# Performance work log

Hardware: AMD Instinct MI355X
Metric: run time of the kernel (lower is better)

The kernel has to match this reference:

```python
import jax, jax.numpy as jnp
import numpy as np

B, L1, L2 = 4, 2048, 2048
INP1_DIM = INP2_DIM = 1024
QK_DIM = V_DIM = 1024
HEAD_N = 16
QK_HEAD = QK_DIM // HEAD_N  # 64
V_HEAD = V_DIM // HEAD_N    # 64
SCALE = 1.0 / (QK_HEAD ** 0.5)


def _linear_params(key, out_dim, in_dim):
    # torch nn.Linear default init: U(-1/sqrt(in), 1/sqrt(in)) for W and b
    kw, kb = jax.random.split(key)
    bound = 1.0 / np.sqrt(in_dim)
    W = jax.random.uniform(kw, (out_dim, in_dim), jnp.float32, -bound, bound)
    b = jax.random.uniform(kb, (out_dim,), jnp.float32, -bound, bound)
    return W, b


def setup_inputs() -> dict:
    key = jax.random.key(0)
    k1, k2, kq, kk, kv = jax.random.split(key, 5)
    inp1 = jax.random.normal(k1, (B, L1, INP1_DIM), jnp.float32)
    inp2 = jax.random.normal(k2, (B, L2, INP2_DIM), jnp.float32)
    Wq, bq = _linear_params(kq, QK_DIM, INP1_DIM)
    Wk, bk = _linear_params(kk, QK_DIM, INP2_DIM)
    Wv, bv = _linear_params(kv, V_DIM, INP2_DIM)
    return {"inp1": inp1, "inp2": inp2, "Wq": Wq, "bq": bq,
            "Wk": Wk, "bk": bk, "Wv": Wv, "bv": bv,
            "rescale_with_score": 1}


def reference(inp1, inp2, Wq, bq, Wk, bk, Wv, bv, rescale_with_score):
    b, l1, _ = inp1.shape
    l2 = inp2.shape[1]
    # torch Linear: x @ W.T + b
    q = (jnp.einsum('bld,ed->ble', inp1, Wq) + bq).reshape(b, l1, HEAD_N, QK_HEAD)
    k = (jnp.einsum('bmd,ed->bme', inp2, Wk) + bk).reshape(b, l2, HEAD_N, QK_HEAD)
    v = (jnp.einsum('bmd,ed->bme', inp2, Wv) + bv).reshape(b, l2, HEAD_N, V_HEAD)
    # scores: [b, l1, l2, h], softmax over l2 (axis=2)
    s = jax.nn.softmax(jnp.einsum('blhd,bmhd->blmh', q, k) * SCALE, axis=2)
    res = jnp.einsum('blmh,bmhd->blhd', s, v)  # [b, l1, h, v_head]
    if rescale_with_score:
        # per-query, per-head sum of squared attention weights -> [b, l1, h, 1]
        denom = jnp.sqrt(jnp.sum(s * s, axis=2))[..., None]
        res = res / denom
    return res.reshape(b, l1, -1)
```

## Files before the change

### kernel.cpp

```cpp
#include <hip/hip_runtime.h>
#include <hip/hip_bf16.h>

#define HEADS   16
#define HD      64
#define DMODEL  1024
#define LQ      2048
#define LK      2048
#define BATCH   4
#define MROWS   8192

typedef __attribute__((ext_vector_type(8))) short short8;
typedef __attribute__((ext_vector_type(4))) float f32x4;
typedef __attribute__((ext_vector_type(16))) float f32x16;
typedef __attribute__((ext_vector_type(2))) unsigned int uint2v;

union V4u { unsigned u[4]; short8 s8; };

static __device__ __forceinline__ unsigned short f2bf(float f) {
  unsigned u = __builtin_bit_cast(unsigned, f);
  u = (u + 0x7FFFu + ((u >> 16) & 1u)) >> 16;
  return (unsigned short)u;
}

static __device__ __forceinline__ unsigned cvtpk(float lo, float hi) {
  unsigned w;
  asm("v_cvt_pk_bf16_f32 %0, %1, %2" : "=v"(w) : "v"(lo), "v"(hi));
  return w;
}

static __device__ __forceinline__ void permswap(unsigned &a, unsigned &b) {
  asm volatile("v_permlane32_swap_b32 %0, %1" : "+v"(a), "+v"(b));
}

static __device__ __forceinline__ void gload_lds16(const void* g, void* l) {
  __builtin_amdgcn_global_load_lds(
      (const __attribute__((address_space(1))) unsigned int*)g,
      (__attribute__((address_space(3))) unsigned int*)l, 16, 0, 0);
}

static __device__ __forceinline__ unsigned lds_addr(const void* p) {
  return (unsigned)(size_t)(const __attribute__((address_space(3))) void*)p;
}

static __device__ __forceinline__ void ds_read128(unsigned addr, V4u &d) {
  asm volatile("ds_read_b128 %0, %1" : "=v"(d.s8) : "v"(addr));
}

static __device__ __forceinline__ void ds_read_tr(unsigned addr, uint2v &d) {
  asm volatile("ds_read_b64_tr_b16 %0, %1" : "=v"(d) : "v"(addr));
}

__global__ void cvt_in_kernel(const float* __restrict__ s0, unsigned short* __restrict__ d0,
                              const float* __restrict__ s1, unsigned short* __restrict__ d1,
                              int n4) {
  int i = blockIdx.x * blockDim.x + threadIdx.x;
  if (i >= n4) return;
  const float* s = blockIdx.y ? s1 : s0;
  unsigned short* d = blockIdx.y ? d1 : d0;
  float4 v = ((const float4*)s)[i];
  ushort4 o;
  o.x = f2bf(v.x); o.y = f2bf(v.y); o.z = f2bf(v.z); o.w = f2bf(v.w);
  ((ushort4*)d)[i] = o;
}

__global__ void cvt_w_kernel(const float* __restrict__ s0, unsigned short* __restrict__ d0,
                             const float* __restrict__ s1, unsigned short* __restrict__ d1,
                             const float* __restrict__ s2, unsigned short* __restrict__ d2,
                             float scale0, int n4) {
  int i = blockIdx.x * blockDim.x + threadIdx.x;
  if (i >= n4) return;
  const float* s = blockIdx.y == 0 ? s0 : (blockIdx.y == 1 ? s1 : s2);
  unsigned short* d = blockIdx.y == 0 ? d0 : (blockIdx.y == 1 ? d1 : d2);
  float sc = blockIdx.y == 0 ? scale0 : 1.0f;
  float4 v = ((const float4*)s)[i];
  ushort4 o;
  o.x = f2bf(v.x * sc); o.y = f2bf(v.y * sc); o.z = f2bf(v.z * sc); o.w = f2bf(v.w * sc);
  ((ushort4*)d)[i] = o;
}

__global__ __launch_bounds__(256, 4) void gemm3_kernel(
    const unsigned short* __restrict__ X1,
    const unsigned short* __restrict__ X2,
    const unsigned short* __restrict__ Wqb,
    const unsigned short* __restrict__ Wkb,
    const unsigned short* __restrict__ Wvb,
    const float* __restrict__ bq,
    const float* __restrict__ bk,
    const float* __restrict__ bv,
    unsigned short* __restrict__ Qb,
    unsigned short* __restrict__ Kb,
    unsigned short* __restrict__ Vb,
    float cexp) {
  __shared__ __attribute__((aligned(16))) unsigned short As[128 * 32];
  __shared__ __attribute__((aligned(16))) unsigned short Bs[128 * 32];
  const int sel = blockIdx.z;
  const unsigned short* A = (sel == 0) ? X1 : X2;
  const unsigned short* W = (sel == 0) ? Wqb : (sel == 1) ? Wkb : Wvb;
  const float* bias = (sel == 0) ? bq : (sel == 1) ? bk : bv;
  unsigned short* C = (sel == 0) ? Qb : (sel == 1) ? Kb : Vb;
  const float bscale = (sel == 0) ? cexp : 1.0f;

  const int tid = threadIdx.x;
  const int l = tid & 63, w = tid >> 6;
  const int c = l & 15, g = l >> 4;
  const int wm = w >> 1, wn = w & 1;
  const int m0 = blockIdx.x * 128, n0 = blockIdx.y * 128;

  f32x4 acc[4][4];
#pragma unroll
  for (int i = 0; i < 4; ++i)
#pragma unroll
    for (int j = 0; j < 4; ++j) acc[i][j] = (f32x4){0.f, 0.f, 0.f, 0.f};

  for (int k0 = 0; k0 < 1024; k0 += 32) {
#pragma unroll
    for (int is = 0; is < 2; ++is) {
      int lin = is * 256 + tid;
      int r = lin >> 2, s = lin & 3;
      int gofs = (s ^ (r & 3)) * 8;
      gload_lds16(A + (size_t)(m0 + r) * 1024 + k0 + gofs,
                  &As[(is * 256 + (tid & ~63)) * 8]);
      gload_lds16(W + (size_t)(n0 + r) * 1024 + k0 + gofs,
                  &Bs[(is * 256 + (tid & ~63)) * 8]);
    }
    __syncthreads();
    short8 af[4], bfr[4];
#pragma unroll
    for (int mt = 0; mt < 4; ++mt) {
      int row = wm * 64 + mt * 16 + c;
      af[mt] = *(const short8*)((const char*)As + row * 64 + ((g ^ (row & 3)) << 4));
    }
#pragma unroll
    for (int nt = 0; nt < 4; ++nt) {
      int row = wn * 64 + nt * 16 + c;
      bfr[nt] = *(const short8*)((const char*)Bs + row * 64 + ((g ^ (row & 3)) << 4));
    }
    __builtin_amdgcn_s_setprio(1);
#pragma unroll
    for (int mt = 0; mt < 4; ++mt)
#pragma unroll
      for (int nt = 0; nt < 4; ++nt)
        acc[mt][nt] = __builtin_amdgcn_mfma_f32_16x16x32_bf16(af[mt], bfr[nt], acc[mt][nt], 0, 0, 0);
    __builtin_amdgcn_s_setprio(0);
    __syncthreads();
  }
  float bv4[4];
#pragma unroll
  for (int nt = 0; nt < 4; ++nt) bv4[nt] = bias[n0 + wn * 64 + nt * 16 + c] * bscale;
#pragma unroll
  for (int mt = 0; mt < 4; ++mt)
#pragma unroll
    for (int nt = 0; nt < 4; ++nt)
#pragma unroll
      for (int r = 0; r < 4; ++r) {
        int m = m0 + wm * 64 + mt * 16 + g * 4 + r;
        int n = n0 + wn * 64 + nt * 16 + c;
        C[(size_t)m * 1024 + n] = f2bf(acc[mt][nt][r] + bv4[nt]);
      }
}

__global__ __launch_bounds__(512) void attn_kernel(
    const unsigned short* __restrict__ Q,
    const unsigned short* __restrict__ K,
    const unsigned short* __restrict__ V,
    float* __restrict__ out,
    const int* __restrict__ rescale_flag) {
  __shared__ __attribute__((aligned(16))) unsigned short Kbuf[2][64 * 64];
  __shared__ __attribute__((aligned(16))) unsigned short Vbuf[2][64 * 64];
  __shared__ float ivLds[8][32];

  const int tid = threadIdx.x;
  const int lane = tid & 63, w = tid >> 6;
  const int l31 = lane & 31, hi = lane >> 5;

  const int gid = blockIdx.x;
  const int xcd = gid & 7;
  const int o = gid >> 3;
  const int bh = xcd * 8 + (o >> 3);
  const int qb = o & 7;
  const int bb = bh >> 4, h = bh & 15;
  const size_t qrowb = (size_t)bb * LQ + qb * 256 + w * 32;

  const int rs = *rescale_flag;

  short8 qf[4];
#pragma unroll
  for (int ks = 0; ks < 4; ++ks)
    qf[ks] = *(const short8*)(Q + (qrowb + l31) * 1024 + h * 64 + ks * 16 + hi * 8);

  const size_t kvbase = (size_t)bb * LK * 1024 + (size_t)h * 64;
  const int k_kv = w * 8 + (lane >> 3);
  const int k_sl = (lane & 7) ^ (lane >> 3);
  const unsigned short* ksrc0 = K + kvbase + (size_t)k_kv * 1024 + k_sl * 8;
  const int v_kv = (w & 3) * 16 + ((lane >> 4) & 1) * 8 + ((lane >> 5) & 1) * 4 + ((lane >> 1) & 3);
  const int v_d  = (w >> 2) * 32 + ((lane >> 3) & 1) * 16 + (lane & 1) * 8;
  const unsigned short* vsrc0 = V + kvbase + (size_t)v_kv * 1024 + v_d;

  unsigned koff[4];
#pragma unroll
  for (int ks = 0; ks < 4; ++ks)
    koff[ks] = (unsigned)(l31 * 128 + ((((ks << 1) | hi) ^ (l31 & 7)) << 4));
  const unsigned kbase0 = lds_addr(&Kbuf[0][0]);
  const unsigned vbase0 = lds_addr(&Vbuf[0][0]);

  f32x16 po[2];
  po[0] = {}; po[1] = {};
  float zacc0 = 0.f, zacc1 = 0.f, s2acc0 = 0.f, s2acc1 = 0.f;

  gload_lds16(ksrc0, &Kbuf[0][w * 512]);
  gload_lds16(vsrc0, &Vbuf[0][w * 512]);
  __syncthreads();

  int cur = 0;
  for (int t = 0; t < LK / 64; ++t) {
    if (t < LK / 64 - 1) {
      gload_lds16(ksrc0 + (size_t)(t + 1) * 65536, &Kbuf[cur ^ 1][w * 512]);
      gload_lds16(vsrc0 + (size_t)(t + 1) * 65536, &Vbuf[cur ^ 1][w * 512]);
    }
    const unsigned kb = kbase0 + (unsigned)(cur * 8192);
    const unsigned vtr = vbase0 + (unsigned)(cur * 8192) + (unsigned)(lane * 8);

#pragma unroll
    for (int s = 0; s < 2; ++s) {
      V4u kfr[4];
#pragma unroll
      for (int ks = 0; ks < 4; ++ks) ds_read128(kb + s * 4096 + koff[ks], kfr[ks]);
      uint2v ta0, ta1, ta2, ta3, tb0, tb1, tb2, tb3;
      {
        const unsigned a0r = vtr + (2 * s) * 1024;
        const unsigned a1r = vtr + (2 * s + 1) * 1024;
        ds_read_tr(a0r, ta0);
        ds_read_tr(a0r + 512, ta1);
        ds_read_tr(a0r + 4096, ta2);
        ds_read_tr(a0r + 4096 + 512, ta3);
        ds_read_tr(a1r, tb0);
        ds_read_tr(a1r + 512, tb1);
        ds_read_tr(a1r + 4096, tb2);
        ds_read_tr(a1r + 4096 + 512, tb3);
      }
      asm volatile("s_waitcnt lgkmcnt(8)" ::: "memory");
      __builtin_amdgcn_sched_barrier(0);
      f32x16 ps = {};
      __builtin_amdgcn_s_setprio(1);
#pragma unroll
      for (int ks = 0; ks < 4; ++ks)
        ps = __builtin_amdgcn_mfma_f32_32x32x16_bf16(kfr[ks].s8, qf[ks], ps, 0, 0, 0);
      __builtin_amdgcn_s_setprio(0);
      float p[16];
#pragma unroll
      for (int r = 0; r < 16; ++r) p[r] = __builtin_amdgcn_exp2f(ps[r]);
      if (rs) {
#pragma unroll
        for (int r = 0; r < 8; ++r) {
          s2acc0 = fmaf(p[2 * r], p[2 * r], s2acc0);
          s2acc1 = fmaf(p[2 * r + 1], p[2 * r + 1], s2acc1);
        }
      } else {
#pragma unroll
        for (int r = 0; r < 8; ++r) {
          zacc0 += p[2 * r];
          zacc1 += p[2 * r + 1];
        }
      }
      unsigned wlo[4], whi[4];
#pragma unroll
      for (int b = 0; b < 4; ++b) {
        wlo[b] = cvtpk(p[4 * b + 0], p[4 * b + 1]);
        whi[b] = cvtpk(p[4 * b + 2], p[4 * b + 3]);
      }
      {
        unsigned a0 = wlo[0], b0 = wlo[1];
        unsigned a1 = whi[0], b1 = whi[1];
        permswap(a0, b0);
        permswap(a1, b1);
        V4u pau; pau.u[0] = a0; pau.u[1] = a1; pau.u[2] = b0; pau.u[3] = b1;
        asm volatile("s_waitcnt lgkmcnt(4)" ::: "memory");
        __builtin_amdgcn_sched_barrier(0);
        V4u v0u, v1u;
        v0u.u[0] = ta0[0]; v0u.u[1] = ta0[1]; v0u.u[2] = ta1[0]; v0u.u[3] = ta1[1];
        v1u.u[0] = ta2[0]; v1u.u[1] = ta2[1]; v1u.u[2] = ta3[0]; v1u.u[3] = ta3[1];
        __builtin_amdgcn_s_setprio(1);
        po[0] = __builtin_amdgcn_mfma_f32_32x32x16_bf16(pau.s8, v0u.s8, po[0], 0, 0, 0);
        po[1] = __builtin_amdgcn_mfma_f32_32x32x16_bf16(pau.s8, v1u.s8, po[1], 0, 0, 0);
        __builtin_amdgcn_s_setprio(0);
      }
      {
        unsigned a0 = wlo[2], b0 = wlo[3];
        unsigned a1 = whi[2], b1 = whi[3];
        permswap(a0, b0);
        permswap(a1, b1);
        V4u pau; pau.u[0] = a0; pau.u[1] = a1; pau.u[2] = b0; pau.u[3] = b1;
        asm volatile("s_waitcnt lgkmcnt(0)" ::: "memory");
        __builtin_amdgcn_sched_barrier(0);
        V4u v0u, v1u;
        v0u.u[0] = tb0[0]; v0u.u[1] = tb0[1]; v0u.u[2] = tb1[0]; v0u.u[3] = tb1[1];
        v1u.u[0] = tb2[0]; v1u.u[1] = tb2[1]; v1u.u[2] = tb3[0]; v1u.u[3] = tb3[1];
        __builtin_amdgcn_s_setprio(1);
        po[0] = __builtin_amdgcn_mfma_f32_32x32x16_bf16(pau.s8, v0u.s8, po[0], 0, 0, 0);
        po[1] = __builtin_amdgcn_mfma_f32_32x32x16_bf16(pau.s8, v1u.s8, po[1], 0, 0, 0);
        __builtin_amdgcn_s_setprio(0);
      }
    }
    __syncthreads();
    cur ^= 1;
  }

  float zacc = zacc0 + zacc1, s2acc = s2acc0 + s2acc1;
  float z2 = zacc + __shfl_xor(zacc, 32, 64);
  float s22 = s2acc + __shfl_xor(s2acc, 32, 64);
  float iv = rs ? (1.0f / sqrtf(s22)) : (1.0f / z2);
  ivLds[w][l31] = iv;

#pragma unroll
  for (int dt = 0; dt < 2; ++dt)
#pragma unroll
    for (int r = 0; r < 16; ++r) {
      const int ql = (r & 3) + 8 * (r >> 2) + 4 * hi;
      out[(qrowb + ql) * 1024 + h * 64 + dt * 32 + l31] = po[dt][r] * ivLds[w][ql];
    }
}

extern "C" void kernel_launch(void* const* d_in, const int* in_sizes, int n_in,
                              void* d_out, int out_size, void* d_ws, size_t ws_size,
                              hipStream_t stream) {
  const float* inp1 = (const float*)d_in[0];
  const float* inp2 = (const float*)d_in[1];
  const float* Wq = (const float*)d_in[2];
  const float* bq = (const float*)d_in[3];
  const float* Wk = (const float*)d_in[4];
  const float* bk = (const float*)d_in[5];
  const float* Wv = (const float*)d_in[6];
  const float* bv = (const float*)d_in[7];
  const int* rs = (const int*)d_in[8];
  float* out = (float*)d_out;

  const float CEXP = 0.18033688011112042f;

  unsigned short* X1  = (unsigned short*)d_ws;
  unsigned short* X2  = X1 + (size_t)MROWS * 1024;
  unsigned short* Wqb = X2 + (size_t)MROWS * 1024;
  unsigned short* Wkb = Wqb + (size_t)1024 * 1024;
  unsigned short* Wvb = Wkb + (size_t)1024 * 1024;
  unsigned short* Qb  = Wvb + (size_t)1024 * 1024;
  unsigned short* Kb  = Qb + (size_t)MROWS * 1024;
  unsigned short* Vb  = Kb + (size_t)MROWS * 1024;

  cvt_in_kernel<<<dim3(MROWS * 1024 / 1024, 2), 256, 0, stream>>>(inp1, X1, inp2, X2, MROWS * 1024 / 4);
  cvt_w_kernel<<<dim3(1024, 3), 256, 0, stream>>>(Wq, Wqb, Wk, Wkb, Wv, Wvb, CEXP, 1024 * 1024 / 4);

  gemm3_kernel<<<dim3(64, 8, 3), 256, 0, stream>>>(X1, X2, Wqb, Wkb, Wvb,
                                                   bq, bk, bv, Qb, Kb, Vb, CEXP);

  attn_kernel<<<dim3(512), 512, 0, stream>>>(Qb, Kb, Vb, out, rs);
}
```

Measured before the change: 162.8 us.

## Halve attention block to 4 waves and fold LDS offsets into immediates

The attention kernel now launches 1024 blocks of 256 threads, each covering 128 query rows instead of 256. Each thread issues twice as many global-to-LDS loads per K/V tile to keep the shared tile the same size. LDS read addresses now use immediate offsets instead of per-read VALU address adds. The smaller blocks give the scheduler more blocks to balance across CUs, but each K/V tile is reused by fewer query rows, which doubles total K/V traffic.

```diff
diff --git a/kernel.cpp b/kernel.cpp
--- a/kernel.cpp
+++ b/kernel.cpp
@@ -42,12 +42,12 @@
   return (unsigned)(size_t)(const __attribute__((address_space(3))) void*)p;
 }
 
-static __device__ __forceinline__ void ds_read128(unsigned addr, V4u &d) {
-  asm volatile("ds_read_b128 %0, %1" : "=v"(d.s8) : "v"(addr));
-}
-
-static __device__ __forceinline__ void ds_read_tr(unsigned addr, uint2v &d) {
-  asm volatile("ds_read_b64_tr_b16 %0, %1" : "=v"(d) : "v"(addr));
+static __device__ __forceinline__ void ds_read128o(unsigned addr, int imm, V4u &d) {
+  asm volatile("ds_read_b128 %0, %1 offset:%c2" : "=v"(d.s8) : "v"(addr), "i"(imm));
+}
+
+static __device__ __forceinline__ void ds_read_tro(unsigned addr, int imm, uint2v &d) {
+  asm volatile("ds_read_b64_tr_b16 %0, %1 offset:%c2" : "=v"(d) : "v"(addr), "i"(imm));
 }
 
 __global__ void cvt_in_kernel(const float* __restrict__ s0, unsigned short* __restrict__ d0,
@@ -159,7 +159,7 @@
       }
 }
 
-__global__ __launch_bounds__(512) void attn_kernel(
+__global__ __launch_bounds__(256) void attn_kernel(
     const unsigned short* __restrict__ Q,
     const unsigned short* __restrict__ K,
     const unsigned short* __restrict__ V,
@@ -167,7 +167,7 @@
     const int* __restrict__ rescale_flag) {
   __shared__ __attribute__((aligned(16))) unsigned short Kbuf[2][64 * 64];
   __shared__ __attribute__((aligned(16))) unsigned short Vbuf[2][64 * 64];
-  __shared__ float ivLds[8][32];
+  __shared__ float ivLds[4][32];
 
   const int tid = threadIdx.x;
   const int lane = tid & 63, w = tid >> 6;
@@ -176,10 +176,10 @@
   const int gid = blockIdx.x;
   const int xcd = gid & 7;
   const int o = gid >> 3;
-  const int bh = xcd * 8 + (o >> 3);
-  const int qb = o & 7;
+  const int bh = xcd * 8 + (o >> 4);
+  const int qb = o & 15;
   const int bb = bh >> 4, h = bh & 15;
-  const size_t qrowb = (size_t)bb * LQ + qb * 256 + w * 32;
+  const size_t qrowb = (size_t)bb * LQ + qb * 128 + w * 32;
 
   const int rs = *rescale_flag;
 
@@ -189,12 +189,14 @@
     qf[ks] = *(const short8*)(Q + (qrowb + l31) * 1024 + h * 64 + ks * 16 + hi * 8);
 
   const size_t kvbase = (size_t)bb * LK * 1024 + (size_t)h * 64;
-  const int k_kv = w * 8 + (lane >> 3);
-  const int k_sl = (lane & 7) ^ (lane >> 3);
+  const int k_kv = tid >> 3;
+  const int k_sl = (tid & 7) ^ (k_kv & 7);
   const unsigned short* ksrc0 = K + kvbase + (size_t)k_kv * 1024 + k_sl * 8;
+  const unsigned short* ksrc1 = ksrc0 + (size_t)32 * 1024;
   const int v_kv = (w & 3) * 16 + ((lane >> 4) & 1) * 8 + ((lane >> 5) & 1) * 4 + ((lane >> 1) & 3);
-  const int v_d  = (w >> 2) * 32 + ((lane >> 3) & 1) * 16 + (lane & 1) * 8;
+  const int v_d  = ((lane >> 3) & 1) * 16 + (lane & 1) * 8;
   const unsigned short* vsrc0 = V + kvbase + (size_t)v_kv * 1024 + v_d;
+  const unsigned short* vsrc1 = vsrc0 + 32;
 
   unsigned koff[4];
 #pragma unroll
@@ -208,36 +210,39 @@
   float zacc0 = 0.f, zacc1 = 0.f, s2acc0 = 0.f, s2acc1 = 0.f;
 
   gload_lds16(ksrc0, &Kbuf[0][w * 512]);
+  gload_lds16(ksrc1, &Kbuf[0][(4 + w) * 512]);
   gload_lds16(vsrc0, &Vbuf[0][w * 512]);
+  gload_lds16(vsrc1, &Vbuf[0][(4 + w) * 512]);
   __syncthreads();
 
   int cur = 0;
   for (int t = 0; t < LK / 64; ++t) {
     if (t < LK / 64 - 1) {
-      gload_lds16(ksrc0 + (size_t)(t + 1) * 65536, &Kbuf[cur ^ 1][w * 512]);
-      gload_lds16(vsrc0 + (size_t)(t + 1) * 65536, &Vbuf[cur ^ 1][w * 512]);
-    }
-    const unsigned kb = kbase0 + (unsigned)(cur * 8192);
+      const size_t adv = (size_t)(t + 1) * 65536;
+      gload_lds16(ksrc0 + adv, &Kbuf[cur ^ 1][w * 512]);
+      gload_lds16(ksrc1 + adv, &Kbuf[cur ^ 1][(4 + w) * 512]);
+      gload_lds16(vsrc0 + adv, &Vbuf[cur ^ 1][w * 512]);
+      gload_lds16(vsrc1 + adv, &Vbuf[cur ^ 1][(4 + w) * 512]);
+    }
+    unsigned kaddr[4];
+#pragma unroll
+    for (int ks = 0; ks < 4; ++ks) kaddr[ks] = kbase0 + (unsigned)(cur * 8192) + koff[ks];
     const unsigned vtr = vbase0 + (unsigned)(cur * 8192) + (unsigned)(lane * 8);
 
 #pragma unroll
     for (int s = 0; s < 2; ++s) {
       V4u kfr[4];
 #pragma unroll
-      for (int ks = 0; ks < 4; ++ks) ds_read128(kb + s * 4096 + koff[ks], kfr[ks]);
+      for (int ks = 0; ks < 4; ++ks) ds_read128o(kaddr[ks], s * 4096, kfr[ks]);
       uint2v ta0, ta1, ta2, ta3, tb0, tb1, tb2, tb3;
-      {
-        const unsigned a0r = vtr + (2 * s) * 1024;
-        const unsigned a1r = vtr + (2 * s + 1) * 1024;
-        ds_read_tr(a0r, ta0);
-        ds_read_tr(a0r + 512, ta1);
-        ds_read_tr(a0r + 4096, ta2);
-        ds_read_tr(a0r + 4096 + 512, ta3);
-        ds_read_tr(a1r, tb0);
-        ds_read_tr(a1r + 512, tb1);
-        ds_read_tr(a1r + 4096, tb2);
-        ds_read_tr(a1r + 4096 + 512, tb3);
-      }
+      ds_read_tro(vtr, (2 * s) * 1024, ta0);
+      ds_read_tro(vtr, (2 * s) * 1024 + 512, ta1);
+      ds_read_tro(vtr, (2 * s) * 1024 + 4096, ta2);
+      ds_read_tro(vtr, (2 * s) * 1024 + 4608, ta3);
+      ds_read_tro(vtr, (2 * s + 1) * 1024, tb0);
+      ds_read_tro(vtr, (2 * s + 1) * 1024 + 512, tb1);
+      ds_read_tro(vtr, (2 * s + 1) * 1024 + 4096, tb2);
+      ds_read_tro(vtr, (2 * s + 1) * 1024 + 4608, tb3);
       asm volatile("s_waitcnt lgkmcnt(8)" ::: "memory");
       __builtin_amdgcn_sched_barrier(0);
       f32x16 ps = {};
@@ -351,5 +356,5 @@
   gemm3_kernel<<<dim3(64, 8, 3), 256, 0, stream>>>(X1, X2, Wqb, Wkb, Wvb,
                                                    bq, bk, bv, Qb, Kb, Vb, CEXP);
 
-  attn_kernel<<<dim3(512), 512, 0, stream>>>(Qb, Kb, Vb, out, rs);
-}
+  attn_kernel<<<dim3(1024), 256, 0, stream>>>(Qb, Kb, Vb, out, rs);
+}
```

After: 174.7 us. 7.3% more time.

## Software-pipeline attention inner loop: issue both QK^T halves before softmax/PV

Applied to the files above, without the earlier changes.

Unrolls the two 32-key sub-steps of each 64-key tile by hand. Both QK^T MFMA groups are issued before the exp/PV work, so the second score MFMA can overlap the first half's softmax and V reads. LDS reads now use immediate offsets to cut address arithmetic, the accumulators are split four ways, and launch bounds request 4 waves per SIMD. The cost is more live registers, with occupancy now bounded by the new launch bound.

```diff
diff --git a/kernel.cpp b/kernel.cpp
--- a/kernel.cpp
+++ b/kernel.cpp
@@ -42,13 +42,15 @@
   return (unsigned)(size_t)(const __attribute__((address_space(3))) void*)p;
 }
 
-static __device__ __forceinline__ void ds_read128(unsigned addr, V4u &d) {
-  asm volatile("ds_read_b128 %0, %1" : "=v"(d.s8) : "v"(addr));
-}
-
-static __device__ __forceinline__ void ds_read_tr(unsigned addr, uint2v &d) {
-  asm volatile("ds_read_b64_tr_b16 %0, %1" : "=v"(d) : "v"(addr));
-}
+static __device__ __forceinline__ void ds_read128o(unsigned addr, int imm, V4u &d) {
+  asm volatile("ds_read_b128 %0, %1 offset:%c2" : "=v"(d.s8) : "v"(addr), "i"(imm));
+}
+
+static __device__ __forceinline__ void ds_read_tro(unsigned addr, int imm, uint2v &d) {
+  asm volatile("ds_read_b64_tr_b16 %0, %1 offset:%c2" : "=v"(d) : "v"(addr), "i"(imm));
+}
+
+#define SB() __builtin_amdgcn_sched_barrier(0)
 
 __global__ void cvt_in_kernel(const float* __restrict__ s0, unsigned short* __restrict__ d0,
                               const float* __restrict__ s1, unsigned short* __restrict__ d1,
@@ -159,7 +161,7 @@
       }
 }
 
-__global__ __launch_bounds__(512) void attn_kernel(
+__global__ __launch_bounds__(512, 4) void attn_kernel(
     const unsigned short* __restrict__ Q,
     const unsigned short* __restrict__ K,
     const unsigned short* __restrict__ V,
@@ -205,7 +207,8 @@
 
   f32x16 po[2];
   po[0] = {}; po[1] = {};
-  float zacc0 = 0.f, zacc1 = 0.f, s2acc0 = 0.f, s2acc1 = 0.f;
+  float za0 = 0.f, za1 = 0.f, za2 = 0.f, za3 = 0.f;
+  float s20 = 0.f, s21 = 0.f, s22a = 0.f, s23 = 0.f;
 
   gload_lds16(ksrc0, &Kbuf[0][w * 512]);
   gload_lds16(vsrc0, &Vbuf[0][w * 512]);
@@ -217,49 +220,62 @@
       gload_lds16(ksrc0 + (size_t)(t + 1) * 65536, &Kbuf[cur ^ 1][w * 512]);
       gload_lds16(vsrc0 + (size_t)(t + 1) * 65536, &Vbuf[cur ^ 1][w * 512]);
     }
-    const unsigned kb = kbase0 + (unsigned)(cur * 8192);
+    unsigned kaddr[4];
+#pragma unroll
+    for (int ks = 0; ks < 4; ++ks) kaddr[ks] = kbase0 + (unsigned)(cur * 8192) + koff[ks];
     const unsigned vtr = vbase0 + (unsigned)(cur * 8192) + (unsigned)(lane * 8);
 
-#pragma unroll
-    for (int s = 0; s < 2; ++s) {
-      V4u kfr[4];
-#pragma unroll
-      for (int ks = 0; ks < 4; ++ks) ds_read128(kb + s * 4096 + koff[ks], kfr[ks]);
-      uint2v ta0, ta1, ta2, ta3, tb0, tb1, tb2, tb3;
-      {
-        const unsigned a0r = vtr + (2 * s) * 1024;
-        const unsigned a1r = vtr + (2 * s + 1) * 1024;
-        ds_read_tr(a0r, ta0);
-        ds_read_tr(a0r + 512, ta1);
-        ds_read_tr(a0r + 4096, ta2);
-        ds_read_tr(a0r + 4096 + 512, ta3);
-        ds_read_tr(a1r, tb0);
-        ds_read_tr(a1r + 512, tb1);
-        ds_read_tr(a1r + 4096, tb2);
-        ds_read_tr(a1r + 4096 + 512, tb3);
-      }
-      asm volatile("s_waitcnt lgkmcnt(8)" ::: "memory");
-      __builtin_amdgcn_sched_barrier(0);
-      f32x16 ps = {};
-      __builtin_amdgcn_s_setprio(1);
-#pragma unroll
-      for (int ks = 0; ks < 4; ++ks)
-        ps = __builtin_amdgcn_mfma_f32_32x32x16_bf16(kfr[ks].s8, qf[ks], ps, 0, 0, 0);
-      __builtin_amdgcn_s_setprio(0);
+    V4u kfr0[4], kfr1[4];
+#pragma unroll
+    for (int ks = 0; ks < 4; ++ks) ds_read128o(kaddr[ks], 0, kfr0[ks]);
+#pragma unroll
+    for (int ks = 0; ks < 4; ++ks) ds_read128o(kaddr[ks], 4096, kfr1[ks]);
+    uint2v ta0, ta1, ta2, ta3, tb0, tb1, tb2, tb3;
+    ds_read_tro(vtr, 0, ta0);
+    ds_read_tro(vtr, 512, ta1);
+    ds_read_tro(vtr, 4096, ta2);
+    ds_read_tro(vtr, 4608, ta3);
+    asm volatile("s_waitcnt lgkmcnt(8)" ::: "memory");
+    SB();
+    f32x16 ps0 = {};
+    __builtin_amdgcn_s_setprio(1);
+    ps0 = __builtin_amdgcn_mfma_f32_32x32x16_bf16(kfr0[0].s8, qf[0], ps0, 0, 0, 0);
+    ps0 = __builtin_amdgcn_mfma_f32_32x32x16_bf16(kfr0[1].s8, qf[1], ps0, 0, 0, 0);
+    ps0 = __builtin_amdgcn_mfma_f32_32x32x16_bf16(kfr0[2].s8, qf[2], ps0, 0, 0, 0);
+    ps0 = __builtin_amdgcn_mfma_f32_32x32x16_bf16(kfr0[3].s8, qf[3], ps0, 0, 0, 0);
+    __builtin_amdgcn_s_setprio(0);
+    SB();
+    ds_read_tro(vtr, 1024, tb0);
+    ds_read_tro(vtr, 1536, tb1);
+    ds_read_tro(vtr, 5120, tb2);
+    ds_read_tro(vtr, 5632, tb3);
+    asm volatile("s_waitcnt lgkmcnt(8)" ::: "memory");
+    SB();
+    f32x16 ps1 = {};
+    __builtin_amdgcn_s_setprio(1);
+    ps1 = __builtin_amdgcn_mfma_f32_32x32x16_bf16(kfr1[0].s8, qf[0], ps1, 0, 0, 0);
+    ps1 = __builtin_amdgcn_mfma_f32_32x32x16_bf16(kfr1[1].s8, qf[1], ps1, 0, 0, 0);
+    ps1 = __builtin_amdgcn_mfma_f32_32x32x16_bf16(kfr1[2].s8, qf[2], ps1, 0, 0, 0);
+    ps1 = __builtin_amdgcn_mfma_f32_32x32x16_bf16(kfr1[3].s8, qf[3], ps1, 0, 0, 0);
+    __builtin_amdgcn_s_setprio(0);
+    SB();
+    {
       float p[16];
 #pragma unroll
-      for (int r = 0; r < 16; ++r) p[r] = __builtin_amdgcn_exp2f(ps[r]);
+      for (int r = 0; r < 16; ++r) p[r] = __builtin_amdgcn_exp2f(ps0[r]);
       if (rs) {
 #pragma unroll
-        for (int r = 0; r < 8; ++r) {
-          s2acc0 = fmaf(p[2 * r], p[2 * r], s2acc0);
-          s2acc1 = fmaf(p[2 * r + 1], p[2 * r + 1], s2acc1);
+        for (int r = 0; r < 4; ++r) {
+          s20 = fmaf(p[4 * r + 0], p[4 * r + 0], s20);
+          s21 = fmaf(p[4 * r + 1], p[4 * r + 1], s21);
+          s22a = fmaf(p[4 * r + 2], p[4 * r + 2], s22a);
+          s23 = fmaf(p[4 * r + 3], p[4 * r + 3], s23);
         }
       } else {
 #pragma unroll
-        for (int r = 0; r < 8; ++r) {
-          zacc0 += p[2 * r];
-          zacc1 += p[2 * r + 1];
+        for (int r = 0; r < 4; ++r) {
+          za0 += p[4 * r + 0]; za1 += p[4 * r + 1];
+          za2 += p[4 * r + 2]; za3 += p[4 * r + 3];
         }
       }
       unsigned wlo[4], whi[4];
@@ -269,13 +285,11 @@
         whi[b] = cvtpk(p[4 * b + 2], p[4 * b + 3]);
       }
       {
-        unsigned a0 = wlo[0], b0 = wlo[1];
-        unsigned a1 = whi[0], b1 = whi[1];
-        permswap(a0, b0);
-        permswap(a1, b1);
+        unsigned a0 = wlo[0], b0 = wlo[1], a1 = whi[0], b1 = whi[1];
+        permswap(a0, b0); permswap(a1, b1);
         V4u pau; pau.u[0] = a0; pau.u[1] = a1; pau.u[2] = b0; pau.u[3] = b1;
         asm volatile("s_waitcnt lgkmcnt(4)" ::: "memory");
-        __builtin_amdgcn_sched_barrier(0);
+        SB();
         V4u v0u, v1u;
         v0u.u[0] = ta0[0]; v0u.u[1] = ta0[1]; v0u.u[2] = ta1[0]; v0u.u[3] = ta1[1];
         v1u.u[0] = ta2[0]; v1u.u[1] = ta2[1]; v1u.u[2] = ta3[0]; v1u.u[3] = ta3[1];
@@ -285,13 +299,11 @@
         __builtin_amdgcn_s_setprio(0);
       }
       {
-        unsigned a0 = wlo[2], b0 = wlo[3];
-        unsigned a1 = whi[2], b1 = whi[3];
-        permswap(a0, b0);
-        permswap(a1, b1);
+        unsigned a0 = wlo[2], b0 = wlo[3], a1 = whi[2], b1 = whi[3];
+        permswap(a0, b0); permswap(a1, b1);
         V4u pau; pau.u[0] = a0; pau.u[1] = a1; pau.u[2] = b0; pau.u[3] = b1;
         asm volatile("s_waitcnt lgkmcnt(0)" ::: "memory");
-        __builtin_amdgcn_sched_barrier(0);
+        SB();
         V4u v0u, v1u;
         v0u.u[0] = tb0[0]; v0u.u[1] = tb0[1]; v0u.u[2] = tb1[0]; v0u.u[3] = tb1[1];
         v1u.u[0] = tb2[0]; v1u.u[1] = tb2[1]; v1u.u[2] = tb3[0]; v1u.u[3] = tb3[1];
@@ -301,11 +313,75 @@
         __builtin_amdgcn_s_setprio(0);
       }
     }
+    uint2v tc0, tc1, tc2, tc3, td0, td1, td2, td3;
+    ds_read_tro(vtr, 2048, tc0);
+    ds_read_tro(vtr, 2560, tc1);
+    ds_read_tro(vtr, 6144, tc2);
+    ds_read_tro(vtr, 6656, tc3);
+    ds_read_tro(vtr, 3072, td0);
+    ds_read_tro(vtr, 3584, td1);
+    ds_read_tro(vtr, 7168, td2);
+    ds_read_tro(vtr, 7680, td3);
+    {
+      float p[16];
+#pragma unroll
+      for (int r = 0; r < 16; ++r) p[r] = __builtin_amdgcn_exp2f(ps1[r]);
+      if (rs) {
+#pragma unroll
+        for (int r = 0; r < 4; ++r) {
+          s20 = fmaf(p[4 * r + 0], p[4 * r + 0], s20);
+          s21 = fmaf(p[4 * r + 1], p[4 * r + 1], s21);
+          s22a = fmaf(p[4 * r + 2], p[4 * r + 2], s22a);
+          s23 = fmaf(p[4 * r + 3], p[4 * r + 3], s23);
+        }
+      } else {
+#pragma unroll
+        for (int r = 0; r < 4; ++r) {
+          za0 += p[4 * r + 0]; za1 += p[4 * r + 1];
+          za2 += p[4 * r + 2]; za3 += p[4 * r + 3];
+        }
+      }
+      unsigned wlo[4], whi[4];
+#pragma unroll
+      for (int b = 0; b < 4; ++b) {
+        wlo[b] = cvtpk(p[4 * b + 0], p[4 * b + 1]);
+        whi[b] = cvtpk(p[4 * b + 2], p[4 * b + 3]);
+      }
+      {
+        unsigned a0 = wlo[0], b0 = wlo[1], a1 = whi[0], b1 = whi[1];
+        permswap(a0, b0); permswap(a1, b1);
+        V4u pau; pau.u[0] = a0; pau.u[1] = a1; pau.u[2] = b0; pau.u[3] = b1;
+        asm volatile("s_waitcnt lgkmcnt(4)" ::: "memory");
+        SB();
+        V4u v0u, v1u;
+        v0u.u[0] = tc0[0]; v0u.u[1] = tc0[1]; v0u.u[2] = tc1[0]; v0u.u[3] = tc1[1];
+        v1u.u[0] = tc2[0]; v1u.u[1] = tc2[1]; v1u.u[2] = tc3[0]; v1u.u[3] = tc3[1];
+        __builtin_amdgcn_s_setprio(1);
+        po[0] = __builtin_amdgcn_mfma_f32_32x32x16_bf16(pau.s8, v0u.s8, po[0], 0, 0, 0);
+        po[1] = __builtin_amdgcn_mfma_f32_32x32x16_bf16(pau.s8, v1u.s8, po[1], 0, 0, 0);
+        __builtin_amdgcn_s_setprio(0);
+      }
+      {
+        unsigned a0 = wlo[2], b0 = wlo[3], a1 = whi[2], b1 = whi[3];
+        permswap(a0, b0); permswap(a1, b1);
+        V4u pau; pau.u[0] = a0; pau.u[1] = a1; pau.u[2] = b0; pau.u[3] = b1;
+        asm volatile("s_waitcnt lgkmcnt(0)" ::: "memory");
+        SB();
+        V4u v0u, v1u;
+        v0u.u[0] = td0[0]; v0u.u[1] = td0[1]; v0u.u[2] = td1[0]; v0u.u[3] = td1[1];
+        v1u.u[0] = td2[0]; v1u.u[1] = td2[1]; v1u.u[2] = td3[0]; v1u.u[3] = td3[1];
+        __builtin_amdgcn_s_setprio(1);
+        po[0] = __builtin_amdgcn_mfma_f32_32x32x16_bf16(pau.s8, v0u.s8, po[0], 0, 0, 0);
+        po[1] = __builtin_amdgcn_mfma_f32_32x32x16_bf16(pau.s8, v1u.s8, po[1], 0, 0, 0);
+        __builtin_amdgcn_s_setprio(0);
+      }
+    }
     __syncthreads();
     cur ^= 1;
   }
 
-  float zacc = zacc0 + zacc1, s2acc = s2acc0 + s2acc1;
+  float zacc = (za0 + za1) + (za2 + za3);
+  float s2acc = (s20 + s21) + (s22a + s23);
   float z2 = zacc + __shfl_xor(zacc, 32, 64);
   float s22 = s2acc + __shfl_xor(s2acc, 32, 64);
   float iv = rs ? (1.0f / sqrtf(s22)) : (1.0f / z2);
```

Result: slower. 166.5 us (+2.2%).
